# Kernel optimization log

Hardware: AMD Instinct MI355X
Metric: run time of the kernel (lower is better)

## Reference

```python
import jax, jax.numpy as jnp
import numpy as np
from jax.ops import segment_sum, segment_max

N_NODES = 50000
N_EDGES = 800000
B = 1024            # number of graphs
NODE_DIM = 21
ESM_DIM = 480
TAB_DIM = 7
H = 128             # hidden_dim
LSTM_H = H // 2     # 64 per direction
NEG_SLOPE = 0.2
BN_EPS = 1e-5


def setup_inputs() -> dict:
    key = jax.random.key(0)
    ks = iter(jax.random.split(key, 48))
    r = lambda shape, s=0.05: (s * jax.random.normal(next(ks), shape)).astype(jnp.float32)
    inp = {
        'x': jax.random.normal(next(ks), (N_NODES, NODE_DIM), dtype=jnp.float32),
        'edge_index': jax.random.randint(next(ks), (2, N_EDGES), 0, N_NODES, dtype=jnp.int64),
        'batch': jnp.sort(jax.random.randint(next(ks), (N_NODES,), 0, B, dtype=jnp.int64)),
        'esm_emb': jax.random.normal(next(ks), (B, ESM_DIM), dtype=jnp.float32),
        'tab_feats': jax.random.normal(next(ks), (B, TAB_DIM), dtype=jnp.float32),
        # GATConv 1 (heads=1)
        'gat1_W': r((H, NODE_DIM)), 'gat1_asrc': r((H,)), 'gat1_adst': r((H,)), 'gat1_b': r((H,)),
        # GATConv 2
        'gat2_W': r((H, H)), 'gat2_asrc': r((H,)), 'gat2_adst': r((H,)), 'gat2_b': r((H,)),
        # Bidirectional LSTM (seq_len=1, so a single cell step per direction)
        'lstm_Wih_f': r((4 * LSTM_H, ESM_DIM)), 'lstm_Whh_f': r((4 * LSTM_H, LSTM_H)),
        'lstm_bih_f': r((4 * LSTM_H,)), 'lstm_bhh_f': r((4 * LSTM_H,)),
        'lstm_Wih_r': r((4 * LSTM_H, ESM_DIM)), 'lstm_Whh_r': r((4 * LSTM_H, LSTM_H)),
        'lstm_bih_r': r((4 * LSTM_H,)), 'lstm_bhh_r': r((4 * LSTM_H,)),
        # tabular net
        'tab_W': r((64, TAB_DIM)), 'tab_b': r((64,)), 'tab_bn_g': jnp.ones((64,), jnp.float32), 'tab_bn_b': jnp.zeros((64,), jnp.float32),
        # fusion head
        'fus1_W': r((256, 320)), 'fus1_b': r((256,)), 'fus_bn_g': jnp.ones((256,), jnp.float32), 'fus_bn_b': jnp.zeros((256,), jnp.float32),
        'fus2_W': r((128, 256)), 'fus2_b': r((128,)),
        'fus3_W': r((1, 128)), 'fus3_b': r((1,)),
    }
    return inp


def _gat(h_in, src, dst, W, a_src, a_dst, bias):
    # PyG GATConv, heads=1, concat=True, self-loops already appended.
    h = h_in @ W.T                                  # [N, H]
    alpha_s = h @ a_src                             # [N]
    alpha_d = h @ a_dst                             # [N]
    e = jax.nn.leaky_relu(alpha_s[src] + alpha_d[dst], NEG_SLOPE)  # [E]
    m = segment_max(e, dst, num_segments=N_NODES)   # stable softmax per target
    ex = jnp.exp(e - m[dst])
    den = segment_sum(ex, dst, num_segments=N_NODES)
    coef = ex / (den[dst] + 1e-16)
    out = segment_sum(coef[:, None] * h[src], dst, num_segments=N_NODES)
    return out + bias


def _bn(x, g, b):
    # BatchNorm1d in training mode: biased batch statistics
    mu = jnp.mean(x, axis=0)
    var = jnp.var(x, axis=0)
    return (x - mu) * jax.lax.rsqrt(var + BN_EPS) * g + b


def _lstm_step(x, Wih, Whh, bih, bhh):
    # single step with zero initial (h, c); Whh term vanishes but kept for fidelity
    g = x @ Wih.T + bih + jnp.zeros((x.shape[0], Whh.shape[1]), x.dtype) @ Whh.T + bhh
    i, f, gg, o = jnp.split(g, 4, axis=1)           # PyTorch gate order i,f,g,o
    c = jax.nn.sigmoid(i) * jnp.tanh(gg)
    return jax.nn.sigmoid(o) * jnp.tanh(c)


def reference(x, edge_index, batch, esm_emb, tab_feats,
              gat1_W, gat1_asrc, gat1_adst, gat1_b,
              gat2_W, gat2_asrc, gat2_adst, gat2_b,
              lstm_Wih_f, lstm_Whh_f, lstm_bih_f, lstm_bhh_f,
              lstm_Wih_r, lstm_Whh_r, lstm_bih_r, lstm_bhh_r,
              tab_W, tab_b, tab_bn_g, tab_bn_b,
              fus1_W, fus1_b, fus_bn_g, fus_bn_b,
              fus2_W, fus2_b, fus3_W, fus3_b):
    sl = jnp.arange(N_NODES, dtype=edge_index.dtype)
    src = jnp.concatenate([edge_index[0], sl])      # add_self_loops=True default
    dst = jnp.concatenate([edge_index[1], sl])

    h1 = jax.nn.relu(_gat(x, src, dst, gat1_W, gat1_asrc, gat1_adst, gat1_b))
    h2 = jax.nn.relu(_gat(h1, src, dst, gat2_W, gat2_asrc, gat2_adst, gat2_b))

    counts = segment_sum(jnp.ones((N_NODES,), h2.dtype), batch, num_segments=B)
    graph_embed = segment_sum(h2, batch, num_segments=B) / jnp.maximum(counts, 1.0)[:, None]

    # bilstm over seq_len=1: output at last (only) step = concat(fwd, bwd)
    h_f = _lstm_step(esm_emb, lstm_Wih_f, lstm_Whh_f, lstm_bih_f, lstm_bhh_f)
    h_r = _lstm_step(esm_emb, lstm_Wih_r, lstm_Whh_r, lstm_bih_r, lstm_bhh_r)
    seq_embed = jnp.concatenate([h_f, h_r], axis=1)  # [B, 128]

    tab_embed = jax.nn.relu(_bn(tab_feats @ tab_W.T + tab_b, tab_bn_g, tab_bn_b))

    z = jnp.concatenate([graph_embed, seq_embed, tab_embed], axis=1)  # [B, 320]
    z = jax.nn.relu(_bn(z @ fus1_W.T + fus1_b, fus_bn_g, fus_bn_b))   # dropout: identity (eval)
    z = jax.nn.relu(z @ fus2_W.T + fus2_b)
    return z @ fus3_W.T + fus3_b                     # [B, 1]
```

## Files before the change

kernel.cpp:

```cpp
#include <hip/hip_runtime.h>
#include <hip/hip_bf16.h>

#define N_NODES 50000
#define N_PAD   50048
#define N_EDGES 800000
#define E_TOT   850000
#define NB      1024
#define ESM_DIM 480
#define HD      128
#define NBUCK   196
#define CAP     5120
#define EPB     3321
#define SC_BLK  256
#define G1_BLK  1563
#define LSTM_BLK 1536
#define BND_BLK 196
#define WC_BLK  16
#define TAB_BLK 4

typedef short short8 __attribute__((ext_vector_type(8)));
typedef unsigned short ushort8 __attribute__((ext_vector_type(8)));
typedef float f32x4 __attribute__((ext_vector_type(4)));

__device__ __forceinline__ float bf2f(unsigned int u) {
    union { unsigned int i; float f; } c; c.i = u << 16; return c.f;
}
__device__ __forceinline__ unsigned short f2bf(float f) {
    union { float f; unsigned int i; } c; c.f = f;
    unsigned int i = c.i;
    return (unsigned short)((i + 0x7FFFu + ((i >> 16) & 1u)) >> 16);
}


__device__ void dev_scatter(const int* __restrict__ ei, int* __restrict__ gcur,
                            int* __restrict__ pairs, int blk) {
    __shared__ int hist[NBUCK];
    int t = threadIdx.x;
    for (int u = t; u < NBUCK; u += 256) hist[u] = 0;
    __syncthreads();
    int e0 = blk * EPB;
    int e1 = (e0 + EPB < E_TOT) ? e0 + EPB : E_TOT;
    for (int e = e0 + t; e < e1; e += 256) {
        int d = (e < N_EDGES) ? ei[N_EDGES + e] : (e - N_EDGES);
        atomicAdd(&hist[d >> 8], 1);
    }
    __syncthreads();
    for (int u = t; u < NBUCK; u += 256) {
        int c = hist[u];
        hist[u] = (c > 0) ? atomicAdd(&gcur[u], c) : 0;
    }
    __syncthreads();
    for (int e = e0 + t; e < e1; e += 256) {
        int s, d;
        if (e < N_EDGES) { s = ei[e]; d = ei[N_EDGES + e]; }
        else             { s = d = e - N_EDGES; }
        int bu = d >> 8;
        int pos = atomicAdd(&hist[bu], 1);
        pairs[bu * CAP + pos] = s | ((d & 255) << 16);
    }
}

__device__ void dev_gat1(const float* __restrict__ X, const float* __restrict__ W,
                         const float* __restrict__ asrc, const float* __restrict__ adst,
                         unsigned short* __restrict__ out,
                         float* __restrict__ alpha_s, float* __restrict__ alpha_d, int blk) {
    __shared__ float Xs[32][23];
    __shared__ float Ws[128][21];
    __shared__ float w_as[21], w_ad[21];
    int t = threadIdx.x;
    int r0 = blk * 32;
    for (int idx = t; idx < 128 * 21; idx += 256) Ws[idx / 21][idx % 21] = W[idx];
    for (int idx = t; idx < 32 * 21; idx += 256) {
        int r = idx / 21, k = idx % 21;
        Xs[r][k] = (r0 + r < N_NODES) ? X[(size_t)(r0 + r) * 21 + k] : 0.f;
    }
    __syncthreads();
    if (t < 21) {
        float sa = 0.f, sd = 0.f;
        for (int f2 = 0; f2 < 128; ++f2) {
            float wv = Ws[f2][t];
            sa += wv * asrc[f2];
            sd += wv * adst[f2];
        }
        w_as[t] = sa; w_ad[t] = sd;
    }
    int f = t & 127, rsub = t >> 7;
    float Wreg[21];
#pragma unroll
    for (int k = 0; k < 21; ++k) Wreg[k] = Ws[f][k];
#pragma unroll 4
    for (int r = rsub; r < 32; r += 2) {
        if (r0 + r >= N_NODES) break;
        float a = 0.f;
#pragma unroll
        for (int k = 0; k < 21; ++k) a += Xs[r][k] * Wreg[k];
        out[(size_t)(r0 + r) * HD + f] = f2bf(a);
    }
    __syncthreads();
    if (t < 32 && r0 + t < N_NODES) {
        float sa = 0.f, sd = 0.f;
#pragma unroll
        for (int k = 0; k < 21; ++k) {
            float xv = Xs[t][k];
            sa += xv * w_as[k];
            sd += xv * w_ad[k];
        }
        alpha_s[r0 + t] = sa;
        alpha_d[r0 + t] = sd;
    }
}

__device__ void dev_gemm_split(const float* __restrict__ X, const float* __restrict__ W1,
                               const float* __restrict__ W2, float* __restrict__ out,
                               int K, int F1, int Ftot, int Kc,
                               int bx, int by, int bz) {
    __shared__ float Xs[16][33];
    __shared__ float Ws[64][33];
    int t = threadIdx.x;
    int r0 = bx * 16;
    int fb = by * 64;
    const float* W = (fb < F1) ? (W1 + (size_t)fb * K) : (W2 + (size_t)(fb - F1) * K);
    int k0 = bz * Kc;
    int f = t & 63, rsub = t >> 6;
    float acc0 = 0.f, acc1 = 0.f, acc2 = 0.f, acc3 = 0.f;
    for (int kc = k0; kc < k0 + Kc; kc += 32) {
        {
            int idx = t * 2, xr = idx >> 5, xk = idx & 31;
            const float2 v = *(const float2*)&X[(size_t)(r0 + xr) * K + kc + xk];
            Xs[xr][xk] = v.x; Xs[xr][xk + 1] = v.y;
        }
        {
            int wf = t >> 2, wk = (t & 3) * 8;
            const float4* p = (const float4*)&W[(size_t)wf * K + kc + wk];
            float4 a = p[0], b = p[1];
            Ws[wf][wk] = a.x; Ws[wf][wk + 1] = a.y; Ws[wf][wk + 2] = a.z; Ws[wf][wk + 3] = a.w;
            Ws[wf][wk + 4] = b.x; Ws[wf][wk + 5] = b.y; Ws[wf][wk + 6] = b.z; Ws[wf][wk + 7] = b.w;
        }
        __syncthreads();
#pragma unroll
        for (int k = 0; k < 32; ++k) {
            float w = Ws[f][k];
            acc0 += Xs[rsub][k] * w;
            acc1 += Xs[rsub + 4][k] * w;
            acc2 += Xs[rsub + 8][k] * w;
            acc3 += Xs[rsub + 12][k] * w;
        }
        __syncthreads();
    }
    atomicAdd(&out[(size_t)(r0 + rsub) * Ftot + fb + f], acc0);
    atomicAdd(&out[(size_t)(r0 + rsub + 4) * Ftot + fb + f], acc1);
    atomicAdd(&out[(size_t)(r0 + rsub + 8) * Ftot + fb + f], acc2);
    atomicAdd(&out[(size_t)(r0 + rsub + 12) * Ftot + fb + f], acc3);
}

__device__ void dev_tab4(const float* __restrict__ tf, const float* __restrict__ W,
                         const float* __restrict__ bias, const float* __restrict__ g,
                         const float* __restrict__ b, float* __restrict__ z, int blk) {
    __shared__ float ssum[16][16];
    __shared__ float ssq[16][16];
    int t = threadIdx.x;
    int rg = t >> 4, jl = t & 15;
    int j = blk * 16 + jl;
    float Wj[7];
#pragma unroll
    for (int k = 0; k < 7; ++k) Wj[k] = W[j * 7 + k];
    float bj = bias[j];
    float s = 0.f, q = 0.f;
    for (int rr = 0; rr < 64; ++rr) {
        int row = rg * 64 + rr;
        const float* xp = &tf[(size_t)row * 7];
        float a = bj;
#pragma unroll
        for (int k = 0; k < 7; ++k) a += xp[k] * Wj[k];
        s += a; q += a * a;
    }
    ssum[rg][jl] = s; ssq[rg][jl] = q;
    __syncthreads();
    for (int off = 8; off; off >>= 1) {
        if (rg < off) { ssum[rg][jl] += ssum[rg + off][jl]; ssq[rg][jl] += ssq[rg + off][jl]; }
        __syncthreads();
    }
    float mu = ssum[0][jl] * (1.f / 1024.f);
    float var = ssq[0][jl] * (1.f / 1024.f) - mu * mu;
    float sc = rsqrtf(var + 1e-5f) * g[j];
    float sh = b[j] - mu * sc;
    for (int rr = 0; rr < 64; ++rr) {
        int row = rg * 64 + rr;
        const float* xp = &tf[(size_t)row * 7];
        float a = bj;
#pragma unroll
        for (int k = 0; k < 7; ++k) a += xp[k] * Wj[k];
        z[(size_t)row * 320 + 256 + j] = fmaxf(a * sc + sh, 0.f);
    }
}

__global__ __launch_bounds__(256) void megaA(
        const int* __restrict__ ei, int* __restrict__ gcur, int* __restrict__ pairs,
        const float* __restrict__ x, const float* __restrict__ gat1_W,
        const float* __restrict__ gat1_as, const float* __restrict__ gat1_ad,
        unsigned short* __restrict__ h0, float* __restrict__ alpha_s, float* __restrict__ alpha_d,
        const float* __restrict__ esm, const float* __restrict__ Wih_f,
        const float* __restrict__ Wih_r, float* __restrict__ g_lstm,
        const int* __restrict__ batch, int* __restrict__ gstart,
        const float* __restrict__ W2, unsigned short* __restrict__ Wb,
        const float* __restrict__ tf, const float* __restrict__ tab_W,
        const float* __restrict__ tab_b, const float* __restrict__ tab_g,
        const float* __restrict__ tab_bb, float* __restrict__ z) {
    int b = blockIdx.x, t = threadIdx.x;
    if (b < SC_BLK) {
        dev_scatter(ei, gcur, pairs, b);
    } else if (b < SC_BLK + G1_BLK) {
        dev_gat1(x, gat1_W, gat1_as, gat1_ad, h0, alpha_s, alpha_d, b - SC_BLK);
    } else if (b < SC_BLK + G1_BLK + LSTM_BLK) {
        int bb = b - (SC_BLK + G1_BLK);
        dev_gemm_split(esm, Wih_f, Wih_r, g_lstm, ESM_DIM, 256, 512, 160,
                       bb & 63, (bb >> 6) & 7, bb >> 9);
    } else if (b < SC_BLK + G1_BLK + LSTM_BLK + BND_BLK) {
        int i = (b - (SC_BLK + G1_BLK + LSTM_BLK)) * 256 + t;
        if (i >= N_NODES) return;
        int bb = batch[i];
        int bp = (i == 0) ? -1 : batch[i - 1];
        for (int g = bp + 1; g <= bb; ++g) gstart[g] = i;
        if (i == N_NODES - 1)
            for (int g = bb + 1; g <= NB; ++g) gstart[g] = N_NODES;
    } else if (b < SC_BLK + G1_BLK + LSTM_BLK + BND_BLK + WC_BLK) {
        int i = (b - (SC_BLK + G1_BLK + LSTM_BLK + BND_BLK)) * 256 + t;
        if (i >= 128 * 32) return;
        float4 v = ((const float4*)W2)[i];
        ((ushort4*)Wb)[i] = make_ushort4(f2bf(v.x), f2bf(v.y), f2bf(v.z), f2bf(v.w));
    } else {
        dev_tab4(tf, tab_W, tab_b, tab_g, tab_bb, z,
                 b - (SC_BLK + G1_BLK + LSTM_BLK + BND_BLK + WC_BLK));
    }
}


__device__ __forceinline__ float sigmoidf_(float x) { return 1.f / (1.f + __expf(-x)); }

__global__ __launch_bounds__(256) void megaB(
        const int* __restrict__ gcur, const int* __restrict__ pairs,
        int* __restrict__ row_beg, int* __restrict__ row_end, int* __restrict__ csr_src,
        const float* __restrict__ g,
        const float* __restrict__ bihf, const float* __restrict__ bhhf,
        const float* __restrict__ bihr, const float* __restrict__ bhhr,
        float* __restrict__ z) {
    int b = blockIdx.x, t = threadIdx.x;
    if (b < NBUCK) {
        __shared__ int dc[256];
        __shared__ int wt[4];
        __shared__ int cur[256];
        int rs = b * CAP;
        int re = rs + gcur[b];
        dc[t] = 0;
        __syncthreads();
        for (int i = rs + t; i < re; i += 256) atomicAdd(&dc[pairs[i] >> 16], 1);
        __syncthreads();
        int v = dc[t];
        int lane = t & 63, wid = t >> 6;
        int sc = v;
#pragma unroll
        for (int off = 1; off < 64; off <<= 1) {
            int n = __shfl_up(sc, off);
            if (lane >= off) sc += n;
        }
        if (lane == 63) wt[wid] = sc;
        __syncthreads();
        int pref = 0;
        for (int ww = 0; ww < wid; ++ww) pref += wt[ww];
        int beg = rs + pref + sc - v;
        int node = b * 256 + t;
        if (node < N_NODES) { row_beg[node] = beg; row_end[node] = beg + v; }
        cur[t] = beg;
        __syncthreads();
        for (int i = rs + t; i < re; i += 256) {
            int pk = pairs[i];
            int pos = atomicAdd(&cur[pk >> 16], 1);
            csr_src[pos] = pk & 0xFFFF;
        }
    } else {
        int idx = (b - NBUCK) * 256 + t;
        if (idx >= NB * 128) return;
        int bb = idx >> 7, jj = idx & 127;
        int dir = jj >> 6, j = jj & 63;
        const float* gb = g + (size_t)bb * 512 + dir * 256;
        const float* bi = dir ? bihr : bihf;
        const float* bh = dir ? bhhr : bhhf;
        float gi = gb[j]       + bi[j]       + bh[j];
        float gg = gb[128 + j] + bi[128 + j] + bh[128 + j];
        float go = gb[192 + j] + bi[192 + j] + bh[192 + j];
        float c = sigmoidf_(gi) * tanhf(gg);
        z[(size_t)bb * 320 + 128 + jj] = sigmoidf_(go) * tanhf(c);
    }
}


__global__ __launch_bounds__(256) void gemm_mfma(const unsigned short* __restrict__ A,
                                                 const unsigned short* __restrict__ Wb,
                                                 const float* __restrict__ asrc,
                                                 const float* __restrict__ adst,
                                                 unsigned short* __restrict__ out,
                                                 float* __restrict__ alpha_s,
                                                 float* __restrict__ alpha_d, int M) {
    __shared__ unsigned short Wlds[128 * 136];
    int t = threadIdx.x;
    for (int u = t; u < 128 * 16; u += 256) {
        int row = u >> 4, seg = u & 15;
        *(ushort8*)&Wlds[row * 136 + seg * 8] = *(const ushort8*)&Wb[row * 128 + seg * 8];
    }
    __syncthreads();
    int wid = t >> 6, L = t & 63;
    int quad = L >> 4, lo = L & 15;
    int m0 = blockIdx.x * 64 + wid * 16;
    short8 afrag[4];
#pragma unroll
    for (int ch = 0; ch < 4; ++ch)
        afrag[ch] = *(const short8*)&A[(size_t)(m0 + lo) * HD + ch * 32 + quad * 8];
    float as_p[4] = {0.f, 0.f, 0.f, 0.f};
    float ad_p[4] = {0.f, 0.f, 0.f, 0.f};
#pragma unroll
    for (int ft = 0; ft < 8; ++ft) {
        f32x4 acc = {0.f, 0.f, 0.f, 0.f};
#pragma unroll
        for (int ch = 0; ch < 4; ++ch) {
            short8 b = *(const short8*)&Wlds[(ft * 16 + lo) * 136 + ch * 32 + quad * 8];
            acc = __builtin_amdgcn_mfma_f32_16x16x32_bf16(afrag[ch], b, acc, 0, 0, 0);
        }
        float asv = asrc[ft * 16 + lo];
        float adv = adst[ft * 16 + lo];
#pragma unroll
        for (int r = 0; r < 4; ++r) {
            int m = m0 + quad * 4 + r;
            if (m < M) out[(size_t)m * HD + ft * 16 + lo] = f2bf(acc[r]);
            as_p[r] += acc[r] * asv;
            ad_p[r] += acc[r] * adv;
        }
    }
#pragma unroll
    for (int off = 1; off < 16; off <<= 1) {
#pragma unroll
        for (int r = 0; r < 4; ++r) {
            as_p[r] += __shfl_xor(as_p[r], off);
            ad_p[r] += __shfl_xor(ad_p[r], off);
        }
    }
    if (lo == 0) {
#pragma unroll
        for (int r = 0; r < 4; ++r) {
            int m = m0 + quad * 4 + r;
            if (m < M) { alpha_s[m] = as_p[r]; alpha_d[m] = ad_p[r]; }
        }
    }
}


__global__ void gat_spmm(const unsigned short* __restrict__ h, const int* __restrict__ row_beg,
                         const int* __restrict__ row_end, const int* __restrict__ csr_src,
                         const float* __restrict__ alpha_s, const float* __restrict__ alpha_d,
                         const float* __restrict__ bias, unsigned short* __restrict__ outp) {
    int w = (int)((blockIdx.x * (size_t)blockDim.x + threadIdx.x) >> 6);
    int lane = threadIdx.x & 63;
    if (w >= N_NODES) return;
    int grp = lane >> 4, l16 = lane & 15;
    int rs = row_beg[w], re = row_end[w];
    int deg = re - rs;
    float ad = alpha_d[w];
    float acc[8] = {0.f, 0.f, 0.f, 0.f, 0.f, 0.f, 0.f, 0.f};
    if (deg <= 64) {
        int s_reg = 0;
        float e = -1e30f;
        if (lane < deg) {
            s_reg = csr_src[rs + lane];
            float t0 = alpha_s[s_reg] + ad;
            e = (t0 > 0.f) ? t0 : 0.2f * t0;
        }
        float m = e;
#pragma unroll
        for (int off = 32; off; off >>= 1) m = fmaxf(m, __shfl_xor(m, off));
        float ex = (lane < deg) ? __expf(e - m) : 0.f;
        float den = ex;
#pragma unroll
        for (int off = 32; off; off >>= 1) den += __shfl_xor(den, off);
        float coef = ex / (den + 1e-16f);
        int i = rs + grp;
        for (; i + 4 < re; i += 8) {
            int idx = i - rs;
            float c0 = __shfl(coef, idx);
            int   s0 = __shfl(s_reg, idx);
            float c1 = __shfl(coef, idx + 4);
            int   s1 = __shfl(s_reg, idx + 4);
            ushort8 h0 = *(const ushort8*)&h[(size_t)s0 * HD + l16 * 8];
            ushort8 h1 = *(const ushort8*)&h[(size_t)s1 * HD + l16 * 8];
#pragma unroll
            for (int j = 0; j < 8; ++j) acc[j] += c0 * bf2f(h0[j]);
#pragma unroll
            for (int j = 0; j < 8; ++j) acc[j] += c1 * bf2f(h1[j]);
        }
        if (i < re) {
            int idx = i - rs;
            float c0 = __shfl(coef, idx);
            int   s0 = __shfl(s_reg, idx);
            ushort8 h0 = *(const ushort8*)&h[(size_t)s0 * HD + l16 * 8];
#pragma unroll
            for (int j = 0; j < 8; ++j) acc[j] += c0 * bf2f(h0[j]);
        }
    } else {
        float m = -1e30f;
        for (int i = rs + lane; i < re; i += 64) {
            int s = csr_src[i];
            float t0 = alpha_s[s] + ad;
            t0 = (t0 > 0.f) ? t0 : 0.2f * t0;
            m = fmaxf(m, t0);
        }
#pragma unroll
        for (int off = 32; off; off >>= 1) m = fmaxf(m, __shfl_xor(m, off));
        float den = 0.f;
        for (int i = rs + lane; i < re; i += 64) {
            int s = csr_src[i];
            float t0 = alpha_s[s] + ad;
            t0 = (t0 > 0.f) ? t0 : 0.2f * t0;
            den += __expf(t0 - m);
        }
#pragma unroll
        for (int off = 32; off; off >>= 1) den += __shfl_xor(den, off);
        float inv = 1.f / (den + 1e-16f);
        for (int i = rs + grp; i < re; i += 4) {
            int s = csr_src[i];
            float t0 = alpha_s[s] + ad;
            t0 = (t0 > 0.f) ? t0 : 0.2f * t0;
            float c = __expf(t0 - m) * inv;
            ushort8 hv = *(const ushort8*)&h[(size_t)s * HD + l16 * 8];
#pragma unroll
            for (int j = 0; j < 8; ++j) acc[j] += c * bf2f(hv[j]);
        }
    }
#pragma unroll
    for (int j = 0; j < 8; ++j) {
        acc[j] += __shfl_xor(acc[j], 16);
        acc[j] += __shfl_xor(acc[j], 32);
    }
    int f0 = l16 * 8 + grp * 2;
    float2 bv = *(const float2*)&bias[f0];
    float vx = fmaxf(acc[grp * 2]     + bv.x, 0.f);
    float vy = fmaxf(acc[grp * 2 + 1] + bv.y, 0.f);
    unsigned int pv = (unsigned int)f2bf(vx) | ((unsigned int)f2bf(vy) << 16);
    *(unsigned int*)&outp[(size_t)w * HD + f0] = pv;
}


__global__ void pool_kernel(const unsigned short* __restrict__ h, const int* __restrict__ start,
                            float* __restrict__ z) {
    int w = (int)((blockIdx.x * (size_t)blockDim.x + threadIdx.x) >> 6);
    int lane = threadIdx.x & 63;
    if (w >= NB) return;
    int grp = lane >> 4, l16 = lane & 15;
    int s0 = start[w], s1 = start[w + 1];
    float acc[8] = {0.f, 0.f, 0.f, 0.f, 0.f, 0.f, 0.f, 0.f};
    int n = s0 + grp;
    for (; n + 4 < s1; n += 8) {
        ushort8 a = *(const ushort8*)&h[(size_t)n * HD + l16 * 8];
        ushort8 b = *(const ushort8*)&h[(size_t)(n + 4) * HD + l16 * 8];
#pragma unroll
        for (int j = 0; j < 8; ++j) acc[j] += bf2f(a[j]);
#pragma unroll
        for (int j = 0; j < 8; ++j) acc[j] += bf2f(b[j]);
    }
    if (n < s1) {
        ushort8 a = *(const ushort8*)&h[(size_t)n * HD + l16 * 8];
#pragma unroll
        for (int j = 0; j < 8; ++j) acc[j] += bf2f(a[j]);
    }
#pragma unroll
    for (int j = 0; j < 8; ++j) {
        acc[j] += __shfl_xor(acc[j], 16);
        acc[j] += __shfl_xor(acc[j], 32);
    }
    float inv = 1.f / fmaxf((float)(s1 - s0), 1.f);
    int f0 = l16 * 8 + grp * 2;
    *(float2*)&z[(size_t)w * 320 + f0] =
        make_float2(acc[grp * 2] * inv, acc[grp * 2 + 1] * inv);
}


__global__ __launch_bounds__(256) void fus1_stats(const float* __restrict__ X,
                                                  const float* __restrict__ W1,
                                                  float* __restrict__ out,
                                                  float* __restrict__ colsum,
                                                  float* __restrict__ colsq) {
    __shared__ float Xs[16][33];
    __shared__ float Ws[64][33];
    __shared__ float cs[4][64];
    __shared__ float cq[4][64];
    int t = threadIdx.x;
    int r0 = blockIdx.x * 16;
    int fb = blockIdx.y * 64;
    const float* W = W1 + (size_t)fb * 320;
    int f = t & 63, rsub = t >> 6;
    float acc0 = 0.f, acc1 = 0.f, acc2 = 0.f, acc3 = 0.f;
    for (int kc = 0; kc < 320; kc += 32) {
// ... 90 lines not shown
        float v = fmaxf(acc[r] + bv, 0.f) * wv;
#pragma unroll
        for (int off = 32; off; off >>= 1) v += __shfl_xor(v, off);
        if ((t & 63) == 0) atomicAdd(&rowsum[rh * 8 + r], v);
    }
    __syncthreads();
    if (t < 16) out[r0 + t] = rowsum[t] + b3[0];
}


extern "C" void kernel_launch(void* const* d_in, const int* in_sizes, int n_in,
                              void* d_out, int out_size, void* d_ws, size_t ws_size,
                              hipStream_t stream) {
    const float* x        = (const float*)d_in[0];
    const int*   ei       = (const int*)d_in[1];
    const int*   batch    = (const int*)d_in[2];
    const float* esm      = (const float*)d_in[3];
    const float* tabf     = (const float*)d_in[4];
    const float* gat1_W   = (const float*)d_in[5];
    const float* gat1_as  = (const float*)d_in[6];
    const float* gat1_ad  = (const float*)d_in[7];
    const float* gat1_b   = (const float*)d_in[8];
    const float* gat2_W   = (const float*)d_in[9];
    const float* gat2_as  = (const float*)d_in[10];
    const float* gat2_ad  = (const float*)d_in[11];
    const float* gat2_b   = (const float*)d_in[12];
    const float* Wih_f    = (const float*)d_in[13];
    const float* bih_f    = (const float*)d_in[15];
    const float* bhh_f    = (const float*)d_in[16];
    const float* Wih_r    = (const float*)d_in[17];
    const float* bih_r    = (const float*)d_in[19];
    const float* bhh_r    = (const float*)d_in[20];
    const float* tab_W    = (const float*)d_in[21];
    const float* tab_b    = (const float*)d_in[22];
    const float* tab_g    = (const float*)d_in[23];
    const float* tab_bb   = (const float*)d_in[24];
    const float* fus1_W   = (const float*)d_in[25];
    const float* fus_g    = (const float*)d_in[27];
    const float* fus_bb   = (const float*)d_in[28];
    const float* fus2_W   = (const float*)d_in[29];
    const float* fus2_b   = (const float*)d_in[30];
    const float* fus3_W   = (const float*)d_in[31];
    const float* fus3_b   = (const float*)d_in[32];
    float* out = (float*)d_out;

    char* ws = (char*)d_ws;
    size_t off = 0;
    auto alloc = [&](size_t bytes) -> char* {
        char* p = ws + off;
        off += (bytes + 255) & ~(size_t)255;
        return p;
    };
    unsigned short* h0_bf = (unsigned short*)alloc((size_t)N_PAD * HD * 2);
    unsigned short* hA_bf = (unsigned short*)alloc((size_t)N_PAD * HD * 2);
    unsigned short* h2_bf = (unsigned short*)alloc((size_t)N_PAD * HD * 2);
    unsigned short* h_act = (unsigned short*)alloc((size_t)N_NODES * HD * 2);
    float* alpha_s = (float*)alloc((size_t)N_NODES * 4);
    float* alpha_d = (float*)alloc((size_t)N_NODES * 4);
    unsigned short* w2bf = (unsigned short*)alloc((size_t)HD * HD * 2);
    int*   row_beg = (int*)alloc((size_t)N_NODES * 4);
    int*   row_end = (int*)alloc((size_t)N_NODES * 4);
    int*   csr_src = (int*)alloc((size_t)NBUCK * CAP * 4);
    int*   pairs   = (int*)alloc((size_t)NBUCK * CAP * 4);
    int*   gstart  = (int*)alloc((size_t)(NB + 1) * 4);
    float* z1pre   = (float*)alloc((size_t)NB * 256 * 4);
    float* z       = (float*)alloc((size_t)NB * 320 * 4);
    float* g_lstm  = (float*)alloc((size_t)NB * 512 * 4);
    int*   gcur    = (int*)alloc((size_t)NBUCK * 4);
    float* colsum  = (float*)alloc((size_t)256 * 4);
    float* colsq   = (float*)alloc((size_t)256 * 4);
    size_t zero_len = (size_t)((char*)colsq + 256 * 4 - (char*)z);
    hipMemsetAsync(z, 0, zero_len, stream);

    megaA<<<SC_BLK + G1_BLK + LSTM_BLK + BND_BLK + WC_BLK + TAB_BLK, 256, 0, stream>>>(
        ei, gcur, pairs, x, gat1_W, gat1_as, gat1_ad, h0_bf, alpha_s, alpha_d,
        esm, Wih_f, Wih_r, g_lstm, batch, gstart, gat2_W, w2bf,
        tabf, tab_W, tab_b, tab_g, tab_bb, z);

    megaB<<<NBUCK + 512, 256, 0, stream>>>(gcur, pairs, row_beg, row_end, csr_src,
                                           g_lstm, bih_f, bhh_f, bih_r, bhh_r, z);

    int aggGrid = (N_NODES + 3) / 4;

    gat_spmm<<<aggGrid, 256, 0, stream>>>(h0_bf, row_beg, row_end, csr_src,
                                          alpha_s, alpha_d, gat1_b, hA_bf);

    gemm_mfma<<<N_PAD / 64, 256, 0, stream>>>(hA_bf, w2bf, gat2_as, gat2_ad,
                                              h2_bf, alpha_s, alpha_d, N_NODES);

    gat_spmm<<<aggGrid, 256, 0, stream>>>(h2_bf, row_beg, row_end, csr_src,
                                          alpha_s, alpha_d, gat2_b, h_act);

    pool_kernel<<<(NB + 3) / 4, 256, 0, stream>>>(h_act, gstart, z);

    fus1_stats<<<dim3(64, 4), 256, 0, stream>>>(z, fus1_W, z1pre, colsum, colsq);

    fus2_final<<<64, 256, 0, stream>>>(z1pre, colsum, colsq, fus_g, fus_bb,
                                       fus2_W, fus2_b, fus3_W, fus3_b, out);

    (void)in_sizes; (void)n_in; (void)out_size; (void)ws_size;
}
```

Measured before the change: 320.3 us.

## Fuse layer-1 GAT aggregation with layer-2 MFMA GEMM via LDS tile

Merges the first gat_spmm and the layer-2 projection GEMM into one kernel. Each block aggregates 64 node rows into an LDS tile and then runs the MFMA GEMM on it, so the intermediate activation never goes through global memory and one launch is removed. Layer-2 alpha values go to separate buffers, because neighbouring blocks still read the layer-1 alphas while this kernel runs. In exchange, the aggregation now runs one block per 64 rows with 16 rows per wave in sequence, which lowers parallelism and latency hiding, and W is read from global/L2 instead of LDS. The scatter block count is also doubled with edges per block halved.

```diff
diff --git a/kernel.cpp b/kernel.cpp
--- a/kernel.cpp
+++ b/kernel.cpp
@@ -10,8 +10,8 @@
 #define HD      128
 #define NBUCK   196
 #define CAP     5120
-#define EPB     3321
-#define SC_BLK  256
+#define SC_BLK  512
+#define EPB     1661
 #define G1_BLK  1563
 #define LSTM_BLK 1536
 #define BND_BLK 196
@@ -294,77 +294,12 @@
 }
 
 
-__global__ __launch_bounds__(256) void gemm_mfma(const unsigned short* __restrict__ A,
-                                                 const unsigned short* __restrict__ Wb,
-                                                 const float* __restrict__ asrc,
-                                                 const float* __restrict__ adst,
-                                                 unsigned short* __restrict__ out,
-                                                 float* __restrict__ alpha_s,
-                                                 float* __restrict__ alpha_d, int M) {
-    __shared__ unsigned short Wlds[128 * 136];
-    int t = threadIdx.x;
-    for (int u = t; u < 128 * 16; u += 256) {
-        int row = u >> 4, seg = u & 15;
-        *(ushort8*)&Wlds[row * 136 + seg * 8] = *(const ushort8*)&Wb[row * 128 + seg * 8];
-    }
-    __syncthreads();
-    int wid = t >> 6, L = t & 63;
-    int quad = L >> 4, lo = L & 15;
-    int m0 = blockIdx.x * 64 + wid * 16;
-    short8 afrag[4];
-#pragma unroll
-    for (int ch = 0; ch < 4; ++ch)
-        afrag[ch] = *(const short8*)&A[(size_t)(m0 + lo) * HD + ch * 32 + quad * 8];
-    float as_p[4] = {0.f, 0.f, 0.f, 0.f};
-    float ad_p[4] = {0.f, 0.f, 0.f, 0.f};
-#pragma unroll
-    for (int ft = 0; ft < 8; ++ft) {
-        f32x4 acc = {0.f, 0.f, 0.f, 0.f};
-#pragma unroll
-        for (int ch = 0; ch < 4; ++ch) {
-            short8 b = *(const short8*)&Wlds[(ft * 16 + lo) * 136 + ch * 32 + quad * 8];
-            acc = __builtin_amdgcn_mfma_f32_16x16x32_bf16(afrag[ch], b, acc, 0, 0, 0);
-        }
-        float asv = asrc[ft * 16 + lo];
-        float adv = adst[ft * 16 + lo];
-#pragma unroll
-        for (int r = 0; r < 4; ++r) {
-            int m = m0 + quad * 4 + r;
-            if (m < M) out[(size_t)m * HD + ft * 16 + lo] = f2bf(acc[r]);
-            as_p[r] += acc[r] * asv;
-            ad_p[r] += acc[r] * adv;
-        }
-    }
-#pragma unroll
-    for (int off = 1; off < 16; off <<= 1) {
-#pragma unroll
-        for (int r = 0; r < 4; ++r) {
-            as_p[r] += __shfl_xor(as_p[r], off);
-            ad_p[r] += __shfl_xor(ad_p[r], off);
-        }
-    }
-    if (lo == 0) {
-#pragma unroll
-        for (int r = 0; r < 4; ++r) {
-            int m = m0 + quad * 4 + r;
-            if (m < M) { alpha_s[m] = as_p[r]; alpha_d[m] = ad_p[r]; }
-        }
-    }
-}
-
-
-__global__ void gat_spmm(const unsigned short* __restrict__ h, const int* __restrict__ row_beg,
-                         const int* __restrict__ row_end, const int* __restrict__ csr_src,
-                         const float* __restrict__ alpha_s, const float* __restrict__ alpha_d,
-                         const float* __restrict__ bias, unsigned short* __restrict__ outp) {
-    int w = (int)((blockIdx.x * (size_t)blockDim.x + threadIdx.x) >> 6);
-    int lane = threadIdx.x & 63;
-    if (w >= N_NODES) return;
-    int grp = lane >> 4, l16 = lane & 15;
-    int rs = row_beg[w], re = row_end[w];
+__device__ __forceinline__ void spmm_row(const unsigned short* __restrict__ h,
+                                         const int* __restrict__ csr_src,
+                                         const float* __restrict__ alpha_s, float ad,
+                                         int rs, int re, int lane, int grp, int l16,
+                                         float acc[8]) {
     int deg = re - rs;
-    float ad = alpha_d[w];
-    float acc[8] = {0.f, 0.f, 0.f, 0.f, 0.f, 0.f, 0.f, 0.f};
     if (deg <= 64) {
         int s_reg = 0;
         float e = -1e30f;
@@ -438,6 +373,91 @@
         acc[j] += __shfl_xor(acc[j], 16);
         acc[j] += __shfl_xor(acc[j], 32);
     }
+}
+
+
+__global__ __launch_bounds__(256) void spmm_gemm(
+        const unsigned short* __restrict__ h, const int* __restrict__ row_beg,
+        const int* __restrict__ row_end, const int* __restrict__ csr_src,
+        const float* __restrict__ alpha_s, const float* __restrict__ alpha_d,
+        const float* __restrict__ bias, const unsigned short* __restrict__ Wb,
+        const float* __restrict__ asrc, const float* __restrict__ adst,
+        unsigned short* __restrict__ h2,
+        float* __restrict__ alpha_s2, float* __restrict__ alpha_d2, int M) {
+    __shared__ unsigned short At[64 * 136];
+    int t = threadIdx.x;
+    int wid = t >> 6, lane = t & 63;
+    int grp = lane >> 4, l16 = lane & 15;
+    int mb = blockIdx.x * 64;
+    int f0 = l16 * 8 + grp * 2;
+    float2 bv = *(const float2*)&bias[f0];
+    for (int r = 0; r < 16; ++r) {
+        int w = mb + wid * 16 + r;
+        unsigned int pv = 0;
+        if (w < N_NODES) {
+            float acc[8] = {0.f, 0.f, 0.f, 0.f, 0.f, 0.f, 0.f, 0.f};
+            spmm_row(h, csr_src, alpha_s, alpha_d[w], row_beg[w], row_end[w],
+                     lane, grp, l16, acc);
+            float vx = fmaxf(acc[grp * 2]     + bv.x, 0.f);
+            float vy = fmaxf(acc[grp * 2 + 1] + bv.y, 0.f);
+            pv = (unsigned int)f2bf(vx) | ((unsigned int)f2bf(vy) << 16);
+        }
+        *(unsigned int*)&At[(wid * 16 + r) * 136 + f0] = pv;
+    }
+    __syncthreads();
+    int quad = grp, lo = l16;
+    short8 afrag[4];
+#pragma unroll
+    for (int ch = 0; ch < 4; ++ch)
+        afrag[ch] = *(const short8*)&At[(wid * 16 + lo) * 136 + ch * 32 + quad * 8];
+    float as_p[4] = {0.f, 0.f, 0.f, 0.f};
+    float ad_p[4] = {0.f, 0.f, 0.f, 0.f};
+#pragma unroll
+    for (int ft = 0; ft < 8; ++ft) {
+        f32x4 acc = {0.f, 0.f, 0.f, 0.f};
+#pragma unroll
+        for (int ch = 0; ch < 4; ++ch) {
+            short8 b = *(const short8*)&Wb[(ft * 16 + lo) * 128 + ch * 32 + quad * 8];
+            acc = __builtin_amdgcn_mfma_f32_16x16x32_bf16(afrag[ch], b, acc, 0, 0, 0);
+        }
+        float asv = asrc[ft * 16 + lo];
+        float adv = adst[ft * 16 + lo];
+#pragma unroll
+        for (int r = 0; r < 4; ++r) {
+            int m = mb + wid * 16 + quad * 4 + r;
+            if (m < M) h2[(size_t)m * HD + ft * 16 + lo] = f2bf(acc[r]);
+            as_p[r] += acc[r] * asv;
+            ad_p[r] += acc[r] * adv;
+        }
+    }
+#pragma unroll
+    for (int off = 1; off < 16; off <<= 1) {
+#pragma unroll
+        for (int r = 0; r < 4; ++r) {
+            as_p[r] += __shfl_xor(as_p[r], off);
+            ad_p[r] += __shfl_xor(ad_p[r], off);
+        }
+    }
+    if (lo == 0) {
+#pragma unroll
+        for (int r = 0; r < 4; ++r) {
+            int m = mb + wid * 16 + quad * 4 + r;
+            if (m < M) { alpha_s2[m] = as_p[r]; alpha_d2[m] = ad_p[r]; }
+        }
+    }
+}
+
+
+__global__ void gat_spmm(const unsigned short* __restrict__ h, const int* __restrict__ row_beg,
+                         const int* __restrict__ row_end, const int* __restrict__ csr_src,
+                         const float* __restrict__ alpha_s, const float* __restrict__ alpha_d,
+                         const float* __restrict__ bias, unsigned short* __restrict__ outp) {
+    int w = (int)((blockIdx.x * (size_t)blockDim.x + threadIdx.x) >> 6);
+    int lane = threadIdx.x & 63;
+    if (w >= N_NODES) return;
+    int grp = lane >> 4, l16 = lane & 15;
+    float acc[8] = {0.f, 0.f, 0.f, 0.f, 0.f, 0.f, 0.f, 0.f};
+    spmm_row(h, csr_src, alpha_s, alpha_d[w], row_beg[w], row_end[w], lane, grp, l16, acc);
     int f0 = l16 * 8 + grp * 2;
     float2 bv = *(const float2*)&bias[f0];
     float vx = fmaxf(acc[grp * 2]     + bv.x, 0.f);
@@ -640,11 +660,12 @@
         return p;
     };
     unsigned short* h0_bf = (unsigned short*)alloc((size_t)N_PAD * HD * 2);
-    unsigned short* hA_bf = (unsigned short*)alloc((size_t)N_PAD * HD * 2);
     unsigned short* h2_bf = (unsigned short*)alloc((size_t)N_PAD * HD * 2);
     unsigned short* h_act = (unsigned short*)alloc((size_t)N_NODES * HD * 2);
-    float* alpha_s = (float*)alloc((size_t)N_NODES * 4);
-    float* alpha_d = (float*)alloc((size_t)N_NODES * 4);
+    float* alpha_s  = (float*)alloc((size_t)N_NODES * 4);
+    float* alpha_d  = (float*)alloc((size_t)N_NODES * 4);
+    float* alpha_s2 = (float*)alloc((size_t)N_NODES * 4);
+    float* alpha_d2 = (float*)alloc((size_t)N_NODES * 4);
     unsigned short* w2bf = (unsigned short*)alloc((size_t)HD * HD * 2);
     int*   row_beg = (int*)alloc((size_t)N_NODES * 4);
     int*   row_end = (int*)alloc((size_t)N_NODES * 4);
@@ -668,16 +689,13 @@
     megaB<<<NBUCK + 512, 256, 0, stream>>>(gcur, pairs, row_beg, row_end, csr_src,
                                            g_lstm, bih_f, bhh_f, bih_r, bhh_r, z);
 
-    int aggGrid = (N_NODES + 3) / 4;
-
-    gat_spmm<<<aggGrid, 256, 0, stream>>>(h0_bf, row_beg, row_end, csr_src,
-                                          alpha_s, alpha_d, gat1_b, hA_bf);
-
-    gemm_mfma<<<N_PAD / 64, 256, 0, stream>>>(hA_bf, w2bf, gat2_as, gat2_ad,
-                                              h2_bf, alpha_s, alpha_d, N_NODES);
-
-    gat_spmm<<<aggGrid, 256, 0, stream>>>(h2_bf, row_beg, row_end, csr_src,
-                                          alpha_s, alpha_d, gat2_b, h_act);
+    spmm_gemm<<<N_PAD / 64, 256, 0, stream>>>(h0_bf, row_beg, row_end, csr_src,
+                                              alpha_s, alpha_d, gat1_b, w2bf,
+                                              gat2_as, gat2_ad, h2_bf,
+                                              alpha_s2, alpha_d2, N_NODES);
+
+    gat_spmm<<<(N_NODES + 3) / 4, 256, 0, stream>>>(h2_bf, row_beg, row_end, csr_src,
+                                                    alpha_s2, alpha_d2, gat2_b, h_act);
 
     pool_kernel<<<(NB + 3) / 4, 256, 0, stream>>>(h_act, gstart, z);
 
```

Result: slower. 346.9 us (+8.3%).

## Compute LSTM input GEMM with bf16 MFMA and fuse LSTM cell into aggregation

Applied to the files above, without the earlier changes.

The LSTM input projection was an fp32 split-K tiled GEMM that accumulated with atomics. It is replaced by a bf16 MFMA GEMM that runs in megaB, fed by new conversion blocks in megaA that cast the ESM embeddings and Wih weights to bf16. The LSTM cell epilogue now runs as extra tail blocks of the first GAT aggregation launch. Other changes: the edge-scatter block count is doubled, intermediate node buffers are reused so one allocation is dropped, and the memset no longer zeroes z or g_lstm because they are no longer written with atomics. The LSTM path loses some precision from bf16 inputs, and it adds conversion traffic and a dependency between the GEMM and the aggregation launch.

```diff
diff --git a/kernel.cpp b/kernel.cpp
--- a/kernel.cpp
+++ b/kernel.cpp
@@ -10,13 +10,15 @@
 #define HD      128
 #define NBUCK   196
 #define CAP     5120
-#define EPB     3321
-#define SC_BLK  256
+#define SC_BLK  512
+#define EPB     1661
 #define G1_BLK  1563
-#define LSTM_BLK 1536
+#define ESMCV_BLK 480
+#define WIHCV_BLK 240
 #define BND_BLK 196
 #define WC_BLK  16
 #define TAB_BLK 4
+#define AGG_BLKS 12500
 
 typedef short short8 __attribute__((ext_vector_type(8)));
 typedef unsigned short ushort8 __attribute__((ext_vector_type(8)));
@@ -110,49 +112,6 @@
     }
 }
 
-__device__ void dev_gemm_split(const float* __restrict__ X, const float* __restrict__ W1,
-                               const float* __restrict__ W2, float* __restrict__ out,
-                               int K, int F1, int Ftot, int Kc,
-                               int bx, int by, int bz) {
-    __shared__ float Xs[16][33];
-    __shared__ float Ws[64][33];
-    int t = threadIdx.x;
-    int r0 = bx * 16;
-    int fb = by * 64;
-    const float* W = (fb < F1) ? (W1 + (size_t)fb * K) : (W2 + (size_t)(fb - F1) * K);
-    int k0 = bz * Kc;
-    int f = t & 63, rsub = t >> 6;
-    float acc0 = 0.f, acc1 = 0.f, acc2 = 0.f, acc3 = 0.f;
-    for (int kc = k0; kc < k0 + Kc; kc += 32) {
-        {
-            int idx = t * 2, xr = idx >> 5, xk = idx & 31;
-            const float2 v = *(const float2*)&X[(size_t)(r0 + xr) * K + kc + xk];
-            Xs[xr][xk] = v.x; Xs[xr][xk + 1] = v.y;
-        }
-        {
-            int wf = t >> 2, wk = (t & 3) * 8;
-            const float4* p = (const float4*)&W[(size_t)wf * K + kc + wk];
-            float4 a = p[0], b = p[1];
-            Ws[wf][wk] = a.x; Ws[wf][wk + 1] = a.y; Ws[wf][wk + 2] = a.z; Ws[wf][wk + 3] = a.w;
-            Ws[wf][wk + 4] = b.x; Ws[wf][wk + 5] = b.y; Ws[wf][wk + 6] = b.z; Ws[wf][wk + 7] = b.w;
-        }
-        __syncthreads();
-#pragma unroll
-        for (int k = 0; k < 32; ++k) {
-            float w = Ws[f][k];
-            acc0 += Xs[rsub][k] * w;
-            acc1 += Xs[rsub + 4][k] * w;
-            acc2 += Xs[rsub + 8][k] * w;
-            acc3 += Xs[rsub + 12][k] * w;
-        }
-        __syncthreads();
-    }
-    atomicAdd(&out[(size_t)(r0 + rsub) * Ftot + fb + f], acc0);
-    atomicAdd(&out[(size_t)(r0 + rsub + 4) * Ftot + fb + f], acc1);
-    atomicAdd(&out[(size_t)(r0 + rsub + 8) * Ftot + fb + f], acc2);
-    atomicAdd(&out[(size_t)(r0 + rsub + 12) * Ftot + fb + f], acc3);
-}
-
 __device__ void dev_tab4(const float* __restrict__ tf, const float* __restrict__ W,
                          const float* __restrict__ bias, const float* __restrict__ g,
                          const float* __restrict__ b, float* __restrict__ z, int blk) {
@@ -199,8 +158,9 @@
         const float* __restrict__ x, const float* __restrict__ gat1_W,
         const float* __restrict__ gat1_as, const float* __restrict__ gat1_ad,
         unsigned short* __restrict__ h0, float* __restrict__ alpha_s, float* __restrict__ alpha_d,
-        const float* __restrict__ esm, const float* __restrict__ Wih_f,
-        const float* __restrict__ Wih_r, float* __restrict__ g_lstm,
+        const float* __restrict__ esm, unsigned short* __restrict__ esm_bf,
+        const float* __restrict__ Wih_f, const float* __restrict__ Wih_r,
+        unsigned short* __restrict__ wih_bf,
         const int* __restrict__ batch, int* __restrict__ gstart,
         const float* __restrict__ W2, unsigned short* __restrict__ Wb,
         const float* __restrict__ tf, const float* __restrict__ tab_W,
@@ -211,39 +171,66 @@
         dev_scatter(ei, gcur, pairs, b);
     } else if (b < SC_BLK + G1_BLK) {
         dev_gat1(x, gat1_W, gat1_as, gat1_ad, h0, alpha_s, alpha_d, b - SC_BLK);
-    } else if (b < SC_BLK + G1_BLK + LSTM_BLK) {
-        int bb = b - (SC_BLK + G1_BLK);
-        dev_gemm_split(esm, Wih_f, Wih_r, g_lstm, ESM_DIM, 256, 512, 160,
-                       bb & 63, (bb >> 6) & 7, bb >> 9);
-    } else if (b < SC_BLK + G1_BLK + LSTM_BLK + BND_BLK) {
-        int i = (b - (SC_BLK + G1_BLK + LSTM_BLK)) * 256 + t;
+    } else if (b < SC_BLK + G1_BLK + ESMCV_BLK) {
+        int i = (b - (SC_BLK + G1_BLK)) * 256 + t;
+        float4 v = ((const float4*)esm)[i];
+        ((ushort4*)esm_bf)[i] = make_ushort4(f2bf(v.x), f2bf(v.y), f2bf(v.z), f2bf(v.w));
+    } else if (b < SC_BLK + G1_BLK + ESMCV_BLK + WIHCV_BLK) {
+        int i = (b - (SC_BLK + G1_BLK + ESMCV_BLK)) * 256 + t;
+        float4 v = (i < 30720) ? ((const float4*)Wih_f)[i] : ((const float4*)Wih_r)[i - 30720];
+        ((ushort4*)wih_bf)[i] = make_ushort4(f2bf(v.x), f2bf(v.y), f2bf(v.z), f2bf(v.w));
+    } else if (b < SC_BLK + G1_BLK + ESMCV_BLK + WIHCV_BLK + BND_BLK) {
+        int i = (b - (SC_BLK + G1_BLK + ESMCV_BLK + WIHCV_BLK)) * 256 + t;
         if (i >= N_NODES) return;
         int bb = batch[i];
         int bp = (i == 0) ? -1 : batch[i - 1];
         for (int g = bp + 1; g <= bb; ++g) gstart[g] = i;
         if (i == N_NODES - 1)
             for (int g = bb + 1; g <= NB; ++g) gstart[g] = N_NODES;
-    } else if (b < SC_BLK + G1_BLK + LSTM_BLK + BND_BLK + WC_BLK) {
-        int i = (b - (SC_BLK + G1_BLK + LSTM_BLK + BND_BLK)) * 256 + t;
+    } else if (b < SC_BLK + G1_BLK + ESMCV_BLK + WIHCV_BLK + BND_BLK + WC_BLK) {
+        int i = (b - (SC_BLK + G1_BLK + ESMCV_BLK + WIHCV_BLK + BND_BLK)) * 256 + t;
         if (i >= 128 * 32) return;
         float4 v = ((const float4*)W2)[i];
         ((ushort4*)Wb)[i] = make_ushort4(f2bf(v.x), f2bf(v.y), f2bf(v.z), f2bf(v.w));
     } else {
         dev_tab4(tf, tab_W, tab_b, tab_g, tab_bb, z,
-                 b - (SC_BLK + G1_BLK + LSTM_BLK + BND_BLK + WC_BLK));
-    }
-}
-
-
-__device__ __forceinline__ float sigmoidf_(float x) { return 1.f / (1.f + __expf(-x)); }
+                 b - (SC_BLK + G1_BLK + ESMCV_BLK + WIHCV_BLK + BND_BLK + WC_BLK));
+    }
+}
+
+
+__device__ void dev_lstm_mfma(const unsigned short* __restrict__ esm_bf,
+                              const unsigned short* __restrict__ wih_bf,
+                              float* __restrict__ g_lstm, int blk) {
+    int t = threadIdx.x;
+    int wid = t >> 6, lane = t & 63;
+    int quad = lane >> 4, lo = lane & 15;
+    int r0 = (blk & 15) * 64 + wid * 16;
+    int fb = (blk >> 4) * 128;
+    short8 afrag[15];
+#pragma unroll
+    for (int ch = 0; ch < 15; ++ch)
+        afrag[ch] = *(const short8*)&esm_bf[(size_t)(r0 + lo) * ESM_DIM + ch * 32 + quad * 8];
+#pragma unroll
+    for (int ft = 0; ft < 8; ++ft) {
+        f32x4 acc = {0.f, 0.f, 0.f, 0.f};
+        const unsigned short* wrow = &wih_bf[(size_t)(fb + ft * 16 + lo) * ESM_DIM + quad * 8];
+#pragma unroll
+        for (int ch = 0; ch < 15; ++ch) {
+            short8 bfr = *(const short8*)&wrow[ch * 32];
+            acc = __builtin_amdgcn_mfma_f32_16x16x32_bf16(afrag[ch], bfr, acc, 0, 0, 0);
+        }
+#pragma unroll
+        for (int r = 0; r < 4; ++r)
+            g_lstm[(size_t)(r0 + quad * 4 + r) * 512 + fb + ft * 16 + lo] = acc[r];
+    }
+}
 
 __global__ __launch_bounds__(256) void megaB(
         const int* __restrict__ gcur, const int* __restrict__ pairs,
         int* __restrict__ row_beg, int* __restrict__ row_end, int* __restrict__ csr_src,
-        const float* __restrict__ g,
-        const float* __restrict__ bihf, const float* __restrict__ bhhf,
-        const float* __restrict__ bihr, const float* __restrict__ bhhr,
-        float* __restrict__ z) {
+        const unsigned short* __restrict__ esm_bf, const unsigned short* __restrict__ wih_bf,
+        float* __restrict__ g_lstm) {
     int b = blockIdx.x, t = threadIdx.x;
     if (b < NBUCK) {
         __shared__ int dc[256];
@@ -278,11 +265,109 @@
             csr_src[pos] = pk & 0xFFFF;
         }
     } else {
-        int idx = (b - NBUCK) * 256 + t;
+        dev_lstm_mfma(esm_bf, wih_bf, g_lstm, b - NBUCK);
+    }
+}
+
+
+__device__ __forceinline__ float sigmoidf_(float x) { return 1.f / (1.f + __expf(-x)); }
+
+__device__ __forceinline__ void spmm_row(const unsigned short* __restrict__ h,
+                                         const int* __restrict__ csr_src,
+                                         const float* __restrict__ alpha_s, float ad,
+                                         int rs, int re, int lane, int grp, int l16,
+                                         float acc[8]) {
+    int deg = re - rs;
+    if (deg <= 64) {
+        int s_reg = 0;
+        float e = -1e30f;
+        if (lane < deg) {
+            s_reg = csr_src[rs + lane];
+            float t0 = alpha_s[s_reg] + ad;
+            e = (t0 > 0.f) ? t0 : 0.2f * t0;
+        }
+        float m = e;
+#pragma unroll
+        for (int off = 32; off; off >>= 1) m = fmaxf(m, __shfl_xor(m, off));
+        float ex = (lane < deg) ? __expf(e - m) : 0.f;
+        float den = ex;
+#pragma unroll
+        for (int off = 32; off; off >>= 1) den += __shfl_xor(den, off);
+        float coef = ex / (den + 1e-16f);
+        int i = rs + grp;
+        for (; i + 4 < re; i += 8) {
+            int idx = i - rs;
+            float c0 = __shfl(coef, idx);
+            int   s0 = __shfl(s_reg, idx);
+            float c1 = __shfl(coef, idx + 4);
+            int   s1 = __shfl(s_reg, idx + 4);
+            ushort8 h0 = *(const ushort8*)&h[(size_t)s0 * HD + l16 * 8];
+            ushort8 h1 = *(const ushort8*)&h[(size_t)s1 * HD + l16 * 8];
+#pragma unroll
+            for (int j = 0; j < 8; ++j) acc[j] += c0 * bf2f(h0[j]);
+#pragma unroll
+            for (int j = 0; j < 8; ++j) acc[j] += c1 * bf2f(h1[j]);
+        }
+        if (i < re) {
+            int idx = i - rs;
+            float c0 = __shfl(coef, idx);
+            int   s0 = __shfl(s_reg, idx);
+            ushort8 h0 = *(const ushort8*)&h[(size_t)s0 * HD + l16 * 8];
+#pragma unroll
+            for (int j = 0; j < 8; ++j) acc[j] += c0 * bf2f(h0[j]);
+        }
+    } else {
+        float m = -1e30f;
+        for (int i = rs + lane; i < re; i += 64) {
+            int s = csr_src[i];
+            float t0 = alpha_s[s] + ad;
+            t0 = (t0 > 0.f) ? t0 : 0.2f * t0;
+            m = fmaxf(m, t0);
+        }
+#pragma unroll
+        for (int off = 32; off; off >>= 1) m = fmaxf(m, __shfl_xor(m, off));
+        float den = 0.f;
+        for (int i = rs + lane; i < re; i += 64) {
+            int s = csr_src[i];
+            float t0 = alpha_s[s] + ad;
+            t0 = (t0 > 0.f) ? t0 : 0.2f * t0;
+            den += __expf(t0 - m);
+        }
+#pragma unroll
+        for (int off = 32; off; off >>= 1) den += __shfl_xor(den, off);
+        float inv = 1.f / (den + 1e-16f);
+        for (int i = rs + grp; i < re; i += 4) {
+            int s = csr_src[i];
+            float t0 = alpha_s[s] + ad;
+            t0 = (t0 > 0.f) ? t0 : 0.2f * t0;
+            float c = __expf(t0 - m) * inv;
+            ushort8 hv = *(const ushort8*)&h[(size_t)s * HD + l16 * 8];
+#pragma unroll
+            for (int j = 0; j < 8; ++j) acc[j] += c * bf2f(hv[j]);
+        }
+    }
+#pragma unroll
+    for (int j = 0; j < 8; ++j) {
+        acc[j] += __shfl_xor(acc[j], 16);
+        acc[j] += __shfl_xor(acc[j], 32);
+    }
+}
+
+
+__global__ void gat_spmm(const unsigned short* __restrict__ h, const int* __restrict__ row_beg,
+                         const int* __restrict__ row_end, const int* __restrict__ csr_src,
+                         const float* __restrict__ alpha_s, const float* __restrict__ alpha_d,
+                         const float* __restrict__ bias, unsigned short* __restrict__ outp,
+                         const float* __restrict__ g_lstm,
+                         const float* __restrict__ bihf, const float* __restrict__ bhhf,
+                         const float* __restrict__ bihr, const float* __restrict__ bhhr,
+                         float* __restrict__ z) {
+    if (blockIdx.x >= AGG_BLKS) {
+        int idx = (blockIdx.x - AGG_BLKS) * 256 + threadIdx.x;
         if (idx >= NB * 128) return;
         int bb = idx >> 7, jj = idx & 127;
         int dir = jj >> 6, j = jj & 63;
-        const float* gb = g + (size_t)bb * 512 + dir * 256;
+        const float* gb = g_lstm + (size_t)bb * 512 + dir * 256;
         const float* bi = dir ? bihr : bihf;
         const float* bh = dir ? bhhr : bhhf;
         float gi = gb[j]       + bi[j]       + bh[j];
@@ -290,7 +375,20 @@
         float go = gb[192 + j] + bi[192 + j] + bh[192 + j];
         float c = sigmoidf_(gi) * tanhf(gg);
         z[(size_t)bb * 320 + 128 + jj] = sigmoidf_(go) * tanhf(c);
-    }
+        return;
+    }
+    int w = (int)((blockIdx.x * (size_t)blockDim.x + threadIdx.x) >> 6);
+    int lane = threadIdx.x & 63;
+    if (w >= N_NODES) return;
+    int grp = lane >> 4, l16 = lane & 15;
+    float acc[8] = {0.f, 0.f, 0.f, 0.f, 0.f, 0.f, 0.f, 0.f};
+    spmm_row(h, csr_src, alpha_s, alpha_d[w], row_beg[w], row_end[w], lane, grp, l16, acc);
+    int f0 = l16 * 8 + grp * 2;
+    float2 bv = *(const float2*)&bias[f0];
+    float vx = fmaxf(acc[grp * 2]     + bv.x, 0.f);
+    float vy = fmaxf(acc[grp * 2 + 1] + bv.y, 0.f);
+    unsigned int pv = (unsigned int)f2bf(vx) | ((unsigned int)f2bf(vy) << 16);
+    *(unsigned int*)&outp[(size_t)w * HD + f0] = pv;
 }
 
 
@@ -350,100 +448,6 @@
             if (m < M) { alpha_s[m] = as_p[r]; alpha_d[m] = ad_p[r]; }
         }
     }
-}
-
-
-__global__ void gat_spmm(const unsigned short* __restrict__ h, const int* __restrict__ row_beg,
-                         const int* __restrict__ row_end, const int* __restrict__ csr_src,
-                         const float* __restrict__ alpha_s, const float* __restrict__ alpha_d,
-                         const float* __restrict__ bias, unsigned short* __restrict__ outp) {
-    int w = (int)((blockIdx.x * (size_t)blockDim.x + threadIdx.x) >> 6);
-    int lane = threadIdx.x & 63;
-    if (w >= N_NODES) return;
-    int grp = lane >> 4, l16 = lane & 15;
-    int rs = row_beg[w], re = row_end[w];
-    int deg = re - rs;
-    float ad = alpha_d[w];
-    float acc[8] = {0.f, 0.f, 0.f, 0.f, 0.f, 0.f, 0.f, 0.f};
-    if (deg <= 64) {
-        int s_reg = 0;
-        float e = -1e30f;
-        if (lane < deg) {
-            s_reg = csr_src[rs + lane];
-            float t0 = alpha_s[s_reg] + ad;
-            e = (t0 > 0.f) ? t0 : 0.2f * t0;
-        }
-        float m = e;
-#pragma unroll
-        for (int off = 32; off; off >>= 1) m = fmaxf(m, __shfl_xor(m, off));
-        float ex = (lane < deg) ? __expf(e - m) : 0.f;
-        float den = ex;
-#pragma unroll
-        for (int off = 32; off; off >>= 1) den += __shfl_xor(den, off);
-        float coef = ex / (den + 1e-16f);
-        int i = rs + grp;
-        for (; i + 4 < re; i += 8) {
-            int idx = i - rs;
-            float c0 = __shfl(coef, idx);
-            int   s0 = __shfl(s_reg, idx);
-            float c1 = __shfl(coef, idx + 4);
-            int   s1 = __shfl(s_reg, idx + 4);
-            ushort8 h0 = *(const ushort8*)&h[(size_t)s0 * HD + l16 * 8];
-            ushort8 h1 = *(const ushort8*)&h[(size_t)s1 * HD + l16 * 8];
-#pragma unroll
-            for (int j = 0; j < 8; ++j) acc[j] += c0 * bf2f(h0[j]);
-#pragma unroll
-            for (int j = 0; j < 8; ++j) acc[j] += c1 * bf2f(h1[j]);
-        }
-        if (i < re) {
-            int idx = i - rs;
-            float c0 = __shfl(coef, idx);
-            int   s0 = __shfl(s_reg, idx);
-            ushort8 h0 = *(const ushort8*)&h[(size_t)s0 * HD + l16 * 8];
-#pragma unroll
-            for (int j = 0; j < 8; ++j) acc[j] += c0 * bf2f(h0[j]);
-        }
-    } else {
-        float m = -1e30f;
-        for (int i = rs + lane; i < re; i += 64) {
-            int s = csr_src[i];
-            float t0 = alpha_s[s] + ad;
-            t0 = (t0 > 0.f) ? t0 : 0.2f * t0;
-            m = fmaxf(m, t0);
-        }
-#pragma unroll
-        for (int off = 32; off; off >>= 1) m = fmaxf(m, __shfl_xor(m, off));
-        float den = 0.f;
-        for (int i = rs + lane; i < re; i += 64) {
-            int s = csr_src[i];
-            float t0 = alpha_s[s] + ad;
-            t0 = (t0 > 0.f) ? t0 : 0.2f * t0;
-            den += __expf(t0 - m);
-        }
-#pragma unroll
-        for (int off = 32; off; off >>= 1) den += __shfl_xor(den, off);
-        float inv = 1.f / (den + 1e-16f);
-        for (int i = rs + grp; i < re; i += 4) {
-            int s = csr_src[i];
-            float t0 = alpha_s[s] + ad;
-            t0 = (t0 > 0.f) ? t0 : 0.2f * t0;
-            float c = __expf(t0 - m) * inv;
-            ushort8 hv = *(const ushort8*)&h[(size_t)s * HD + l16 * 8];
-#pragma unroll
-            for (int j = 0; j < 8; ++j) acc[j] += c * bf2f(hv[j]);
-        }
-    }
-#pragma unroll
-    for (int j = 0; j < 8; ++j) {
-        acc[j] += __shfl_xor(acc[j], 16);
-        acc[j] += __shfl_xor(acc[j], 32);
-    }
-    int f0 = l16 * 8 + grp * 2;
-    float2 bv = *(const float2*)&bias[f0];
-    float vx = fmaxf(acc[grp * 2]     + bv.x, 0.f);
-    float vy = fmaxf(acc[grp * 2 + 1] + bv.y, 0.f);
-    unsigned int pv = (unsigned int)f2bf(vx) | ((unsigned int)f2bf(vy) << 16);
-    *(unsigned int*)&outp[(size_t)w * HD + f0] = pv;
 }
 
 
@@ -640,44 +644,45 @@
         return p;
     };
     unsigned short* h0_bf = (unsigned short*)alloc((size_t)N_PAD * HD * 2);
-    unsigned short* hA_bf = (unsigned short*)alloc((size_t)N_PAD * HD * 2);
     unsigned short* h2_bf = (unsigned short*)alloc((size_t)N_PAD * HD * 2);
     unsigned short* h_act = (unsigned short*)alloc((size_t)N_NODES * HD * 2);
-    float* alpha_s = (float*)alloc((size_t)N_NODES * 4);
-    float* alpha_d = (float*)alloc((size_t)N_NODES * 4);
-    unsigned short* w2bf = (unsigned short*)alloc((size_t)HD * HD * 2);
+    float* alpha_s  = (float*)alloc((size_t)N_NODES * 4);
+    float* alpha_d  = (float*)alloc((size_t)N_NODES * 4);
+    unsigned short* w2bf   = (unsigned short*)alloc((size_t)HD * HD * 2);
+    unsigned short* esm_bf = (unsigned short*)alloc((size_t)NB * ESM_DIM * 2);
+    unsigned short* wih_bf = (unsigned short*)alloc((size_t)512 * ESM_DIM * 2);
+    float* g_lstm  = (float*)alloc((size_t)NB * 512 * 4);
     int*   row_beg = (int*)alloc((size_t)N_NODES * 4);
     int*   row_end = (int*)alloc((size_t)N_NODES * 4);
     int*   csr_src = (int*)alloc((size_t)NBUCK * CAP * 4);
     int*   pairs   = (int*)alloc((size_t)NBUCK * CAP * 4);
     int*   gstart  = (int*)alloc((size_t)(NB + 1) * 4);
+    float* z       = (float*)alloc((size_t)NB * 320 * 4);
     float* z1pre   = (float*)alloc((size_t)NB * 256 * 4);
-    float* z       = (float*)alloc((size_t)NB * 320 * 4);
-    float* g_lstm  = (float*)alloc((size_t)NB * 512 * 4);
     int*   gcur    = (int*)alloc((size_t)NBUCK * 4);
     float* colsum  = (float*)alloc((size_t)256 * 4);
     float* colsq   = (float*)alloc((size_t)256 * 4);
-    size_t zero_len = (size_t)((char*)colsq + 256 * 4 - (char*)z);
-    hipMemsetAsync(z, 0, zero_len, stream);
-
-    megaA<<<SC_BLK + G1_BLK + LSTM_BLK + BND_BLK + WC_BLK + TAB_BLK, 256, 0, stream>>>(
+    size_t zero_len = (size_t)((char*)colsq + 256 * 4 - (char*)gcur);
+    hipMemsetAsync(gcur, 0, zero_len, stream);
+
+    megaA<<<SC_BLK + G1_BLK + ESMCV_BLK + WIHCV_BLK + BND_BLK + WC_BLK + TAB_BLK, 256, 0, stream>>>(
         ei, gcur, pairs, x, gat1_W, gat1_as, gat1_ad, h0_bf, alpha_s, alpha_d,
-        esm, Wih_f, Wih_r, g_lstm, batch, gstart, gat2_W, w2bf,
+        esm, esm_bf, Wih_f, Wih_r, wih_bf, batch, gstart, gat2_W, w2bf,
         tabf, tab_W, tab_b, tab_g, tab_bb, z);
 
-    megaB<<<NBUCK + 512, 256, 0, stream>>>(gcur, pairs, row_beg, row_end, csr_src,
-                                           g_lstm, bih_f, bhh_f, bih_r, bhh_r, z);
-
-    int aggGrid = (N_NODES + 3) / 4;
-
-    gat_spmm<<<aggGrid, 256, 0, stream>>>(h0_bf, row_beg, row_end, csr_src,
-                                          alpha_s, alpha_d, gat1_b, hA_bf);
-
-    gemm_mfma<<<N_PAD / 64, 256, 0, stream>>>(hA_bf, w2bf, gat2_as, gat2_ad,
-                                              h2_bf, alpha_s, alpha_d, N_NODES);
-
-    gat_spmm<<<aggGrid, 256, 0, stream>>>(h2_bf, row_beg, row_end, csr_src,
-                                          alpha_s, alpha_d, gat2_b, h_act);
+    megaB<<<NBUCK + 64, 256, 0, stream>>>(gcur, pairs, row_beg, row_end, csr_src,
+                                          esm_bf, wih_bf, g_lstm);
+
+    gat_spmm<<<AGG_BLKS + 512, 256, 0, stream>>>(h0_bf, row_beg, row_end, csr_src,
+                                                 alpha_s, alpha_d, gat1_b, h2_bf ,
+                                                 g_lstm, bih_f, bhh_f, bih_r, bhh_r, z);
+
+    gemm_mfma<<<N_PAD / 64, 256, 0, stream>>>(h2_bf, w2bf, gat2_as, gat2_ad,
+                                              h0_bf, alpha_s, alpha_d, N_NODES);
+
+    gat_spmm<<<AGG_BLKS, 256, 0, stream>>>(h0_bf, row_beg, row_end, csr_src,
+                                           alpha_s, alpha_d, gat2_b, h_act,
+                                           nullptr, nullptr, nullptr, nullptr, nullptr, nullptr);
 
     pool_kernel<<<(NB + 3) / 4, 256, 0, stream>>>(h_act, gstart, z);
 
```

After: 321.0 us. About the same (+0.2%).
